# Kernel optimization log

Measured on AMD Instinct MI355X. Metric: run time of the kernel, lower is better.

Reference implementation:

```python
import jax, jax.numpy as jnp
import numpy as np

TABLE_LEN = 1_000_000   # embedding rows (n)
EMB_DIM   = 64          # embedding_size (m)
N_BAGS    = 16_384      # batch of bags
BAG_LEN   = 50          # avg indices per bag
N_IDX     = N_BAGS * BAG_LEN


def setup_inputs() -> dict:
    key = jax.random.key(0)
    kw, ki = jax.random.split(key)
    bound = 1.0 / np.sqrt(TABLE_LEN)
    # weight ~ U(-sqrt(1/n), sqrt(1/n)) as in the torch module
    W = jax.random.uniform(kw, (TABLE_LEN, EMB_DIM), jnp.float32, -bound, bound)
    indices = jax.random.randint(ki, (N_IDX,), 0, TABLE_LEN, dtype=jnp.int32)
    # offsets: start index of each bag; bags of uniform length BAG_LEN
    offsets = jnp.arange(N_BAGS, dtype=jnp.int32) * BAG_LEN
    return {"W": W, "indices": indices, "offsets": offsets}


def reference(W, indices, offsets):
    # EmbeddingBag mode='sum': out[b] = sum_{i in bag b} W[indices[i]]
    n_idx = indices.shape[0]
    n_bags = offsets.shape[0]
    # segment id of each index position: which bag it falls into
    seg = jnp.searchsorted(offsets, jnp.arange(n_idx, dtype=offsets.dtype), side="right") - 1
    gathered = W[indices]  # [N_IDX, EMB_DIM]
    out = jax.ops.segment_sum(gathered, seg, num_segments=n_bags)  # [N_BAGS, EMB_DIM]
    return out
```

## Files before the change

### kernel.cpp

```cpp
#include <hip/hip_runtime.h>
#include <hip/hip_bf16.h>


#define EMB 64

__global__ __launch_bounds__(256) void embag_sum_kernel(
    const float* __restrict__ W,
    const int* __restrict__ indices,
    const int* __restrict__ offsets,
    float* __restrict__ out,
    int n_bags, int n_idx)
{
    const int wave = (int)((blockIdx.x * blockDim.x + threadIdx.x) >> 6);
    const int lane = (int)(threadIdx.x & 63);
    if (wave >= n_bags) return;

    const int start = offsets[wave];
    const int end   = (wave + 1 < n_bags) ? offsets[wave + 1] : n_idx;

    float acc0 = 0.f, acc1 = 0.f, acc2 = 0.f, acc3 = 0.f;

    for (int base = start; base < end; base += 64) {
        const int rem = end - base;
        const int cnt = rem < 64 ? rem : 64;
        const int myIdx = (lane < cnt) ? indices[base + lane] : 0;

        int k = 0;
        for (; k + 3 < cnt; k += 4) {
            const unsigned i0 = (unsigned)__shfl(myIdx, k,     64);
            const unsigned i1 = (unsigned)__shfl(myIdx, k + 1, 64);
            const unsigned i2 = (unsigned)__shfl(myIdx, k + 2, 64);
            const unsigned i3 = (unsigned)__shfl(myIdx, k + 3, 64);
            const float w0 = W[i0 * EMB + lane];
            const float w1 = W[i1 * EMB + lane];
            const float w2 = W[i2 * EMB + lane];
            const float w3 = W[i3 * EMB + lane];
            acc0 += w0; acc1 += w1; acc2 += w2; acc3 += w3;
        }
        for (; k < cnt; ++k) {
            const unsigned i = (unsigned)__shfl(myIdx, k, 64);
            acc0 += W[i * EMB + lane];
        }
    }

    out[(unsigned)wave * EMB + lane] = (acc0 + acc1) + (acc2 + acc3);
}

extern "C" void kernel_launch(void* const* d_in, const int* in_sizes, int n_in,
                              void* d_out, int out_size, void* d_ws, size_t ws_size,
                              hipStream_t stream) {
    const float* W        = (const float*)d_in[0];
    const int*   indices  = (const int*)d_in[1];
    const int*   offsets  = (const int*)d_in[2];
    float*       out      = (float*)d_out;

    const int n_idx  = in_sizes[1];
    const int n_bags = in_sizes[2];

    const int waves_per_block = 256 / 64;
    const int n_blocks = (n_bags + waves_per_block - 1) / waves_per_block;

    embag_sum_kernel<<<n_blocks, 256, 0, stream>>>(W, indices, offsets, out,
                                                   n_bags, n_idx);
}
```

Measured before the change: 325.7 us.

## Use float4 loads with four rows per wave and cross-slot shuffle reduction

Each wave now splits into four 16-lane slots, and each lane loads a float4 slice of an embedding row. One wave-wide load instruction therefore fetches four different rows instead of one, which is meant to cut instruction count and keep more independent gathers in flight. Out-of-range rows are read (at index 0) but masked out of the accumulation. Partial sums are combined with xor shuffles before 16 lanes store float4 outputs.

```diff
diff --git a/kernel.cpp b/kernel.cpp
--- a/kernel.cpp
+++ b/kernel.cpp
@@ -15,35 +15,60 @@
     const int lane = (int)(threadIdx.x & 63);
     if (wave >= n_bags) return;
 
+    const int slot = lane >> 4;
+    const int cg   = lane & 15;
+
     const int start = offsets[wave];
     const int end   = (wave + 1 < n_bags) ? offsets[wave + 1] : n_idx;
 
-    float acc0 = 0.f, acc1 = 0.f, acc2 = 0.f, acc3 = 0.f;
+    float4 acc0 = {0.f,0.f,0.f,0.f}, acc1 = {0.f,0.f,0.f,0.f};
+    float4 acc2 = {0.f,0.f,0.f,0.f}, acc3 = {0.f,0.f,0.f,0.f};
 
     for (int base = start; base < end; base += 64) {
         const int rem = end - base;
         const int cnt = rem < 64 ? rem : 64;
         const int myIdx = (lane < cnt) ? indices[base + lane] : 0;
 
-        int k = 0;
-        for (; k + 3 < cnt; k += 4) {
-            const unsigned i0 = (unsigned)__shfl(myIdx, k,     64);
-            const unsigned i1 = (unsigned)__shfl(myIdx, k + 1, 64);
-            const unsigned i2 = (unsigned)__shfl(myIdx, k + 2, 64);
-            const unsigned i3 = (unsigned)__shfl(myIdx, k + 3, 64);
-            const float w0 = W[i0 * EMB + lane];
-            const float w1 = W[i1 * EMB + lane];
-            const float w2 = W[i2 * EMB + lane];
-            const float w3 = W[i3 * EMB + lane];
-            acc0 += w0; acc1 += w1; acc2 += w2; acc3 += w3;
-        }
-        for (; k < cnt; ++k) {
-            const unsigned i = (unsigned)__shfl(myIdx, k, 64);
-            acc0 += W[i * EMB + lane];
+        for (int k = 0; k < cnt; k += 16) {
+            const int r0 = k      + slot;
+            const int r1 = k + 4  + slot;
+            const int r2 = k + 8  + slot;
+            const int r3 = k + 12 + slot;
+            const unsigned i0 = (unsigned)__shfl(myIdx, r0, 64);
+            const unsigned i1 = (unsigned)__shfl(myIdx, r1, 64);
+            const unsigned i2 = (unsigned)__shfl(myIdx, r2, 64);
+            const unsigned i3 = (unsigned)__shfl(myIdx, r3, 64);
+
+            const float4 v0 = *(const float4*)(W + (size_t)i0 * EMB + cg * 4);
+            const float4 v1 = *(const float4*)(W + (size_t)i1 * EMB + cg * 4);
+            const float4 v2 = *(const float4*)(W + (size_t)i2 * EMB + cg * 4);
+            const float4 v3 = *(const float4*)(W + (size_t)i3 * EMB + cg * 4);
+
+            if (r0 < cnt) { acc0.x += v0.x; acc0.y += v0.y; acc0.z += v0.z; acc0.w += v0.w; }
+            if (r1 < cnt) { acc1.x += v1.x; acc1.y += v1.y; acc1.z += v1.z; acc1.w += v1.w; }
+            if (r2 < cnt) { acc2.x += v2.x; acc2.y += v2.y; acc2.z += v2.z; acc2.w += v2.w; }
+            if (r3 < cnt) { acc3.x += v3.x; acc3.y += v3.y; acc3.z += v3.z; acc3.w += v3.w; }
         }
     }
 
-    out[(unsigned)wave * EMB + lane] = (acc0 + acc1) + (acc2 + acc3);
+    float4 acc;
+    acc.x = (acc0.x + acc1.x) + (acc2.x + acc3.x);
+    acc.y = (acc0.y + acc1.y) + (acc2.y + acc3.y);
+    acc.z = (acc0.z + acc1.z) + (acc2.z + acc3.z);
+    acc.w = (acc0.w + acc1.w) + (acc2.w + acc3.w);
+
+    acc.x += __shfl_xor(acc.x, 16, 64);
+    acc.y += __shfl_xor(acc.y, 16, 64);
+    acc.z += __shfl_xor(acc.z, 16, 64);
+    acc.w += __shfl_xor(acc.w, 16, 64);
+    acc.x += __shfl_xor(acc.x, 32, 64);
+    acc.y += __shfl_xor(acc.y, 32, 64);
+    acc.z += __shfl_xor(acc.z, 32, 64);
+    acc.w += __shfl_xor(acc.w, 32, 64);
+
+    if (lane < 16) {
+        *(float4*)(out + (size_t)wave * EMB + lane * 4) = acc;
+    }
 }
 
 extern "C" void kernel_launch(void* const* d_in, const int* in_sizes, int n_in,
```

Result: no change. 325.9 us (+0.1%).
